# Kernel tuning notes

Hardware: AMD Instinct MI355X
Metric: run time of the kernel (lower is better)

Reference implementation:

```python
import jax, jax.numpy as jnp
import numpy as np

N_ENT = 100000
EMBED_DIM = 128
N_EDGES = 3200000
SPARSE_THRESHOLD = 5


def setup_inputs() -> dict:
    key = jax.random.key(0)
    k1, k2, k3, k4 = jax.random.split(key, 4)
    entity_embeds = jax.random.normal(k1, (N_ENT, EMBED_DIM), dtype=jnp.float32)
    node_degrees = jax.random.randint(k2, (N_ENT,), 0, 40, dtype=jnp.int64)
    path_rows = jnp.sort(jax.random.randint(k3, (N_EDGES,), 0, N_ENT, dtype=jnp.int64))
    path_cols = jax.random.randint(k4, (N_EDGES,), 0, N_ENT, dtype=jnp.int64)
    return {
        "entity_embeds": entity_embeds,
        "node_degrees": node_degrees,
        "path_rows": path_rows,
        "path_cols": path_cols,
    }


def reference(entity_embeds, node_degrees, path_rows, path_cols):
    N, dim = entity_embeds.shape
    # node_edge_count = scatter_add(ones, rows), clamped to >= 1
    ones = jnp.ones(path_rows.shape[0], dtype=entity_embeds.dtype)
    node_edge_count = jax.ops.segment_sum(ones, path_rows, num_segments=N)
    node_edge_count = jnp.clip(node_edge_count, 1.0, None)
    # SpMM: remote[i] = sum over path edges (i -> j) of entity_embeds[j]
    gathered = entity_embeds[path_cols]  # [E, dim] (fused into segment_sum by XLA)
    remote = jax.ops.segment_sum(gathered, path_rows, num_segments=N)
    # degree-normalize then mask to sparse (low-degree) nodes only
    remote = remote / node_edge_count[:, None]
    sparse_mask = (node_degrees <= SPARSE_THRESHOLD).astype(entity_embeds.dtype)
    remote = remote * sparse_mask[:, None]
    return remote
```

## Files before the change

kernel.cpp:

```cpp
#include <hip/hip_runtime.h>

#define N_ENT 100000
#define EMBED_DIM 128
#define SPARSE_THRESHOLD 5
#define ROWS_PER_BLOCK 8

__global__ void seg_bounds_kernel(const int* __restrict__ rows,
                                  int* __restrict__ row_start,
                                  int n_edges) {
    int e = blockIdx.x * blockDim.x + threadIdx.x;
    const int stride = gridDim.x * blockDim.x;
    for (; e < n_edges; e += stride) {
        const int r  = rows[e];
        const int rp = (e == 0) ? -1 : rows[e - 1];
        for (int q = rp + 1; q <= r; ++q) row_start[q] = e;
        if (e == n_edges - 1) {
            for (int q = r + 1; q <= N_ENT; ++q) row_start[q] = n_edges;
        }
    }
}

__global__ __launch_bounds__(256) void path_agg_kernel(
    const float4* __restrict__ embeds4,
    const int*    __restrict__ degrees,
    const int*    __restrict__ row_start,
    const int*    __restrict__ cols,
    float4*       __restrict__ out4)
{
    const int sub  = threadIdx.x >> 5;
    const int lane = threadIdx.x & 31;
    const int row  = blockIdx.x * ROWS_PER_BLOCK + sub;

    float4* orow = out4 + (size_t)row * 32;

    if (degrees[row] > SPARSE_THRESHOLD) {
        orow[lane] = make_float4(0.f, 0.f, 0.f, 0.f);
        return;
    }

    const int start = row_start[row];
    const int end   = row_start[row + 1];

    float4 acc = make_float4(0.f, 0.f, 0.f, 0.f);
    int e = start;
    for (; e + 4 <= end; e += 4) {
        const int c0 = cols[e + 0];
        const int c1 = cols[e + 1];
        const int c2 = cols[e + 2];
        const int c3 = cols[e + 3];
        float4 v0 = embeds4[(size_t)c0 * 32 + lane];
        float4 v1 = embeds4[(size_t)c1 * 32 + lane];
        float4 v2 = embeds4[(size_t)c2 * 32 + lane];
        float4 v3 = embeds4[(size_t)c3 * 32 + lane];
        acc.x += v0.x; acc.y += v0.y; acc.z += v0.z; acc.w += v0.w;
        acc.x += v1.x; acc.y += v1.y; acc.z += v1.z; acc.w += v1.w;
        acc.x += v2.x; acc.y += v2.y; acc.z += v2.z; acc.w += v2.w;
        acc.x += v3.x; acc.y += v3.y; acc.z += v3.z; acc.w += v3.w;
    }
    for (; e < end; ++e) {
        const int c = cols[e];
        float4 v = embeds4[(size_t)c * 32 + lane];
        acc.x += v.x; acc.y += v.y; acc.z += v.z; acc.w += v.w;
    }

    const int cnt = end - start;
    const float inv = 1.0f / (float)(cnt > 0 ? cnt : 1);
    acc.x *= inv; acc.y *= inv; acc.z *= inv; acc.w *= inv;
    orow[lane] = acc;
}

__global__ __launch_bounds__(EMBED_DIM) void path_agg_bsearch_kernel(
    const float* __restrict__ embeds,
    const int*   __restrict__ degrees,
    const int*   __restrict__ rows,
    const int*   __restrict__ cols,
    float*       __restrict__ out,
    int n_edges)
{
    const int row = blockIdx.x;
    const int t   = threadIdx.x;
    float* orow = out + (size_t)row * EMBED_DIM;

    if (degrees[row] > SPARSE_THRESHOLD) { orow[t] = 0.0f; return; }

    int lo = 0, hi = n_edges;
    while (lo < hi) { int mid = (lo + hi) >> 1; if (rows[mid] < row) lo = mid + 1; else hi = mid; }
    const int start = lo;
    hi = n_edges;
    while (lo < hi) { int mid = (lo + hi) >> 1; if (rows[mid] <= row) lo = mid + 1; else hi = mid; }
    const int end = lo;

    float acc = 0.0f;
    for (int e = start; e < end; ++e)
        acc += embeds[(size_t)cols[e] * EMBED_DIM + t];

    const int cnt = end - start;
    orow[t] = acc / (float)(cnt > 0 ? cnt : 1);
}

extern "C" void kernel_launch(void* const* d_in, const int* in_sizes, int n_in,
                              void* d_out, int out_size, void* d_ws, size_t ws_size,
                              hipStream_t stream) {
    const float* embeds  = (const float*)d_in[0];
    const int*   degrees = (const int*)d_in[1];
    const int*   rows    = (const int*)d_in[2];
    const int*   cols    = (const int*)d_in[3];
    float* out = (float*)d_out;
    const int n_edges = in_sizes[2];

    const size_t needed = (size_t)(N_ENT + 1) * sizeof(int);
    if (ws_size >= needed) {
        int* row_start = (int*)d_ws;
        seg_bounds_kernel<<<1024, 256, 0, stream>>>(rows, row_start, n_edges);
        path_agg_kernel<<<N_ENT / ROWS_PER_BLOCK, 256, 0, stream>>>(
            (const float4*)embeds, degrees, row_start, cols, (float4*)out);
    } else {
        path_agg_bsearch_kernel<<<N_ENT, EMBED_DIM, 0, stream>>>(
            embeds, degrees, rows, cols, out, n_edges);
    }
}
```

Before: 155.6 us.

## Compact sparse rows into a worklist and zero-fill output separately

The aggregation now runs over a compacted list of low-degree rows, built with an atomic counter, so that waves stop idling on rows masked to zero (about 85% of rows). A separate grid-stride kernel zero-fills the whole output first. The segment-bounds pass now reads rows as int4 and also does the compaction. This adds an extra kernel launch, a second write to the sparse rows, and atomic contention on one counter, and it drops the binary-search fallback when the workspace is small.

```diff
diff --git a/kernel.cpp b/kernel.cpp
--- a/kernel.cpp
+++ b/kernel.cpp
@@ -3,7 +3,110 @@
 #define N_ENT 100000
 #define EMBED_DIM 128
 #define SPARSE_THRESHOLD 5
-#define ROWS_PER_BLOCK 8
+
+#define WS_ROWSTART_OFF 64
+#define WS_LIST_OFF     (64 + ((N_ENT + 1 + 63) & ~63))
+#define WS_NEEDED_INTS  (WS_LIST_OFF + N_ENT)
+
+__global__ __launch_bounds__(256) void zero_fill_kernel(float4* __restrict__ out4,
+                                                        int* __restrict__ counter,
+                                                        int n4) {
+    if (blockIdx.x == 0 && threadIdx.x == 0) *counter = 0;
+    const float4 z = make_float4(0.f, 0.f, 0.f, 0.f);
+    int i = blockIdx.x * blockDim.x + threadIdx.x;
+    const int stride = gridDim.x * blockDim.x;
+    for (; i < n4; i += stride) out4[i] = z;
+}
+
+__global__ __launch_bounds__(256) void bounds_compact_kernel(
+    const int* __restrict__ rows,
+    const int* __restrict__ degrees,
+    int* __restrict__ row_start,
+    int* __restrict__ sparse_list,
+    int* __restrict__ counter,
+    int n_edges)
+{
+    const int tid = blockIdx.x * blockDim.x + threadIdx.x;
+    const int nthreads = gridDim.x * blockDim.x;
+
+    const int4* rows4 = (const int4*)rows;
+    const int n_quads = n_edges >> 2;
+    for (int q = tid; q < n_quads; q += nthreads) {
+        const int e0 = q << 2;
+        const int4 v = rows4[q];
+        const int prev = (e0 == 0) ? -1 : rows[e0 - 1];
+        int rp = prev;
+        const int rv[4] = {v.x, v.y, v.z, v.w};
+        #pragma unroll
+        for (int k = 0; k < 4; ++k) {
+            const int e = e0 + k;
+            const int r = rv[k];
+            for (int qq = rp + 1; qq <= r; ++qq) row_start[qq] = e;
+            if (e == n_edges - 1)
+                for (int qq = r + 1; qq <= N_ENT; ++qq) row_start[qq] = n_edges;
+            rp = r;
+        }
+    }
+    for (int e = (n_quads << 2) + tid; e < n_edges; e += nthreads) {
+        const int r  = rows[e];
+        const int rp = (e == 0) ? -1 : rows[e - 1];
+        for (int qq = rp + 1; qq <= r; ++qq) row_start[qq] = e;
+        if (e == n_edges - 1)
+            for (int qq = r + 1; qq <= N_ENT; ++qq) row_start[qq] = n_edges;
+    }
+
+    for (int r = tid; r < N_ENT; r += nthreads) {
+        if (degrees[r] <= SPARSE_THRESHOLD) {
+            const int pos = atomicAdd(counter, 1);
+            sparse_list[pos] = r;
+        }
+    }
+}
+
+__global__ __launch_bounds__(256) void agg_sparse_kernel(
+    const float4* __restrict__ embeds4,
+    const int*    __restrict__ row_start,
+    const int*    __restrict__ cols,
+    const int*    __restrict__ sparse_list,
+    const int*    __restrict__ counter,
+    float4*       __restrict__ out4)
+{
+    const int nsparse = *counter;
+    const int sub  = threadIdx.x >> 5;
+    const int lane = threadIdx.x & 31;
+
+    for (int idx = blockIdx.x * 8 + sub; idx < nsparse; idx += gridDim.x * 8) {
+        const int row   = sparse_list[idx];
+        const int start = row_start[row];
+        const int end   = row_start[row + 1];
+
+        float4 acc = make_float4(0.f, 0.f, 0.f, 0.f);
+        int e = start;
+        for (; e + 4 <= end; e += 4) {
+            const int c0 = cols[e + 0];
+            const int c1 = cols[e + 1];
+            const int c2 = cols[e + 2];
+            const int c3 = cols[e + 3];
+            float4 v0 = embeds4[(size_t)c0 * 32 + lane];
+            float4 v1 = embeds4[(size_t)c1 * 32 + lane];
+            float4 v2 = embeds4[(size_t)c2 * 32 + lane];
+            float4 v3 = embeds4[(size_t)c3 * 32 + lane];
+            acc.x += v0.x; acc.y += v0.y; acc.z += v0.z; acc.w += v0.w;
+            acc.x += v1.x; acc.y += v1.y; acc.z += v1.z; acc.w += v1.w;
+            acc.x += v2.x; acc.y += v2.y; acc.z += v2.z; acc.w += v2.w;
+            acc.x += v3.x; acc.y += v3.y; acc.z += v3.z; acc.w += v3.w;
+        }
+        for (; e < end; ++e) {
+            float4 v = embeds4[(size_t)cols[e] * 32 + lane];
+            acc.x += v.x; acc.y += v.y; acc.z += v.z; acc.w += v.w;
+        }
+
+        const int cnt = end - start;
+        const float inv = 1.0f / (float)(cnt > 0 ? cnt : 1);
+        acc.x *= inv; acc.y *= inv; acc.z *= inv; acc.w *= inv;
+        out4[(size_t)row * 32 + lane] = acc;
+    }
+}
 
 __global__ void seg_bounds_kernel(const int* __restrict__ rows,
                                   int* __restrict__ row_start,
@@ -14,9 +117,8 @@
         const int r  = rows[e];
         const int rp = (e == 0) ? -1 : rows[e - 1];
         for (int q = rp + 1; q <= r; ++q) row_start[q] = e;
-        if (e == n_edges - 1) {
+        if (e == n_edges - 1)
             for (int q = r + 1; q <= N_ENT; ++q) row_start[q] = n_edges;
-        }
     }
 }
 
@@ -29,73 +131,24 @@
 {
     const int sub  = threadIdx.x >> 5;
     const int lane = threadIdx.x & 31;
-    const int row  = blockIdx.x * ROWS_PER_BLOCK + sub;
+    const int row  = blockIdx.x * 8 + sub;
 
     float4* orow = out4 + (size_t)row * 32;
-
     if (degrees[row] > SPARSE_THRESHOLD) {
         orow[lane] = make_float4(0.f, 0.f, 0.f, 0.f);
         return;
     }
-
     const int start = row_start[row];
     const int end   = row_start[row + 1];
-
     float4 acc = make_float4(0.f, 0.f, 0.f, 0.f);
-    int e = start;
-    for (; e + 4 <= end; e += 4) {
-        const int c0 = cols[e + 0];
-        const int c1 = cols[e + 1];
-        const int c2 = cols[e + 2];
-        const int c3 = cols[e + 3];
-        float4 v0 = embeds4[(size_t)c0 * 32 + lane];
-        float4 v1 = embeds4[(size_t)c1 * 32 + lane];
-        float4 v2 = embeds4[(size_t)c2 * 32 + lane];
-        float4 v3 = embeds4[(size_t)c3 * 32 + lane];
-        acc.x += v0.x; acc.y += v0.y; acc.z += v0.z; acc.w += v0.w;
-        acc.x += v1.x; acc.y += v1.y; acc.z += v1.z; acc.w += v1.w;
-        acc.x += v2.x; acc.y += v2.y; acc.z += v2.z; acc.w += v2.w;
-        acc.x += v3.x; acc.y += v3.y; acc.z += v3.z; acc.w += v3.w;
-    }
-    for (; e < end; ++e) {
-        const int c = cols[e];
-        float4 v = embeds4[(size_t)c * 32 + lane];
+    for (int e = start; e < end; ++e) {
+        float4 v = embeds4[(size_t)cols[e] * 32 + lane];
         acc.x += v.x; acc.y += v.y; acc.z += v.z; acc.w += v.w;
     }
-
     const int cnt = end - start;
     const float inv = 1.0f / (float)(cnt > 0 ? cnt : 1);
     acc.x *= inv; acc.y *= inv; acc.z *= inv; acc.w *= inv;
     orow[lane] = acc;
-}
-
-__global__ __launch_bounds__(EMBED_DIM) void path_agg_bsearch_kernel(
-    const float* __restrict__ embeds,
-    const int*   __restrict__ degrees,
-    const int*   __restrict__ rows,
-    const int*   __restrict__ cols,
-    float*       __restrict__ out,
-    int n_edges)
-{
-    const int row = blockIdx.x;
-    const int t   = threadIdx.x;
-    float* orow = out + (size_t)row * EMBED_DIM;
-
-    if (degrees[row] > SPARSE_THRESHOLD) { orow[t] = 0.0f; return; }
-
-    int lo = 0, hi = n_edges;
-    while (lo < hi) { int mid = (lo + hi) >> 1; if (rows[mid] < row) lo = mid + 1; else hi = mid; }
-    const int start = lo;
-    hi = n_edges;
-    while (lo < hi) { int mid = (lo + hi) >> 1; if (rows[mid] <= row) lo = mid + 1; else hi = mid; }
-    const int end = lo;
-
-    float acc = 0.0f;
-    for (int e = start; e < end; ++e)
-        acc += embeds[(size_t)cols[e] * EMBED_DIM + t];
-
-    const int cnt = end - start;
-    orow[t] = acc / (float)(cnt > 0 ? cnt : 1);
 }
 
 extern "C" void kernel_launch(void* const* d_in, const int* in_sizes, int n_in,
@@ -108,14 +161,22 @@
     float* out = (float*)d_out;
     const int n_edges = in_sizes[2];
 
-    const size_t needed = (size_t)(N_ENT + 1) * sizeof(int);
-    if (ws_size >= needed) {
+    if (ws_size >= (size_t)WS_NEEDED_INTS * sizeof(int)) {
+        int* wsi        = (int*)d_ws;
+        int* counter    = wsi;
+        int* row_start  = wsi + WS_ROWSTART_OFF;
+        int* sparse_list= wsi + WS_LIST_OFF;
+
+        zero_fill_kernel<<<2048, 256, 0, stream>>>((float4*)out, counter, N_ENT * 32);
+        bounds_compact_kernel<<<2048, 256, 0, stream>>>(rows, degrees, row_start,
+                                                        sparse_list, counter, n_edges);
+        agg_sparse_kernel<<<2048, 256, 0, stream>>>((const float4*)embeds, row_start,
+                                                    cols, sparse_list, counter,
+                                                    (float4*)out);
+    } else if (ws_size >= (size_t)(N_ENT + 1) * sizeof(int)) {
         int* row_start = (int*)d_ws;
         seg_bounds_kernel<<<1024, 256, 0, stream>>>(rows, row_start, n_edges);
-        path_agg_kernel<<<N_ENT / ROWS_PER_BLOCK, 256, 0, stream>>>(
+        path_agg_kernel<<<N_ENT / 8, 256, 0, stream>>>(
             (const float4*)embeds, degrees, row_start, cols, (float4*)out);
-    } else {
-        path_agg_bsearch_kernel<<<N_ENT, EMBED_DIM, 0, stream>>>(
-            embeds, degrees, rows, cols, out, n_edges);
     }
 }
```

Result: slower. 168.8 us (+8.5%).
